# Optimization experiments

Hardware: AMD Instinct MI355X
Metric: run time of the kernel (lower is better)

Reference implementation:

```python
import jax, jax.numpy as jnp
import numpy as np

BITS = 4
MAXQ = 15           # 2**BITS - 1
PACK = 32 // BITS   # 8 nibbles per int32
GROUP = 128         # quantization group size along in_features


def _unpack_rows(packed, rows):
    """Unpack int32-packed 4-bit values along axis 0. packed: [Kp, N] -> [rows, N]."""
    shifts = jnp.arange(0, 32, BITS, dtype=jnp.int32)            # [PACK]
    u = (packed[:, None, :] >> shifts[None, :, None]) & MAXQ    # [Kp, PACK, N]
    return u.reshape(-1, packed.shape[1])[:rows]


def _unpack_cols(packed, cols):
    """Unpack int32-packed 4-bit values along axis 1. packed: [G, Np] -> [G, cols]."""
    shifts = jnp.arange(0, 32, BITS, dtype=jnp.int32)            # [PACK]
    u = (packed[:, :, None] >> shifts[None, None, :]) & MAXQ    # [G, Np, PACK]
    return u.reshape(packed.shape[0], -1)[:, :cols]


def setup_inputs() -> dict:
    key = jax.random.key(0)
    k1, k2, k3, k4, k5 = jax.random.split(key, 5)
    K, N = 4096, 11008
    x = jax.random.normal(k1, (4, 2048, K), dtype=jnp.float32)
    qweight = jax.random.randint(k2, (K // PACK, N), 0, 2**31 - 1, dtype=jnp.int32)
    scales = jax.random.uniform(k3, (K // GROUP, N), dtype=jnp.float32)
    qzeros = jax.random.randint(k4, (K // GROUP, (N + PACK - 1) // PACK), 0, 2**31 - 1, dtype=jnp.int32)
    bias = jax.random.normal(k5, (N,), dtype=jnp.float32)
    return {"x": x, "qweight": qweight, "scales": scales, "qzeros": qzeros, "bias": bias}


def reference(x, qweight, scales, qzeros, bias):
    K = x.shape[-1]
    N = scales.shape[1]
    qw = _unpack_rows(qweight, K)            # [K, N] int in [0, 15]
    qz = _unpack_cols(qzeros, N) + 1         # [G, N] int in [1, 16] (+1 per get_unpacked_params)
    s = jnp.repeat(scales, GROUP, axis=0)    # [K, N]  groupwise -> per-row
    z = jnp.repeat(qz, GROUP, axis=0)        # [K, N]
    W = (qw - z).astype(x.dtype) * s         # dequantized weight [K, N]
    out = jnp.matmul(x, W) + bias
    return out.astype(x.dtype)
```

## Files before the change

kernel.cpp:

```cpp
#include <hip/hip_runtime.h>
#include <hip/hip_bf16.h>
#include <stdint.h>

typedef __attribute__((ext_vector_type(4))) float f32x4;
typedef __attribute__((ext_vector_type(8))) short bf16x8;
typedef __attribute__((ext_vector_type(8))) unsigned short ushort8;
typedef __attribute__((ext_vector_type(4))) unsigned short ushort4v;

__device__ __forceinline__ unsigned short f2bf(float f) {
    union { float f; unsigned int u; } v; v.f = f;
    unsigned int u = v.u;
    u += 0x7FFFu + ((u >> 16) & 1u);
    return (unsigned short)(u >> 16);
}

__device__ __forceinline__ int swz(int row, int k) {
    return (row * 64 + k) ^ ((row & 7) << 3);
}

__device__ __forceinline__ void gld16(const void* g, void* l) {
    __builtin_amdgcn_global_load_lds(
        (const __attribute__((address_space(1))) unsigned int*)g,
        (__attribute__((address_space(3))) unsigned int*)l,
        16, 0, 0);
}

__global__ __launch_bounds__(256)
void prep(const float* __restrict__ X, const int* __restrict__ QW,
          const float* __restrict__ SC, const int* __restrict__ QZ,
          unsigned short* __restrict__ Xb, unsigned short* __restrict__ WT,
          int N, int K, long long n8, int deqB) {
    const int bid = blockIdx.x;
    const int t = threadIdx.x;
    if (bid < deqB) {
        const int ntiles = N >> 6;
        const int nb = bid % ntiles;
        const int kb = bid / ntiles;
        const int n0 = nb * 64, kp0 = kb * 64;
        #pragma unroll
        for (int w = 0; w < 16; ++w) {
            const int p = t + 256 * w;
            const int kpo = p & 63, ni = p >> 6;
            const int n = n0 + ni, kp = kp0 + kpo;
            const int g = kp >> 4;
            const float s = SC[(size_t)g * N + n];
            const int zq = ((QZ[(size_t)g * (N >> 3) + (n >> 3)] >> ((n & 7) * 4)) & 15) + 1;
            const float zb = -(float)zq * s;
            const unsigned int q = (unsigned int)QW[(size_t)kp * N + n];
            ushort8 o;
            #pragma unroll
            for (int j = 0; j < 8; ++j)
                o[j] = f2bf(fmaf((float)((q >> (4 * j)) & 15u), s, zb));
            *reinterpret_cast<ushort8*>(&WT[(size_t)n * K + kp * 8]) = o;
        }
    } else {
        long long i0 = (long long)(bid - deqB) * 256 + t;
        long long stride = (long long)(gridDim.x - deqB) * 256;
        for (long long i = i0; i < n8; i += stride) {
            const float4* p = reinterpret_cast<const float4*>(X + i * 8);
            float4 a = p[0], b = p[1];
            ushort8 o;
            o[0] = f2bf(a.x); o[1] = f2bf(a.y); o[2] = f2bf(a.z); o[3] = f2bf(a.w);
            o[4] = f2bf(b.x); o[5] = f2bf(b.y); o[6] = f2bf(b.z); o[7] = f2bf(b.w);
            *reinterpret_cast<ushort8*>(Xb + i * 8) = o;
        }
    }
}

__global__ __launch_bounds__(256)
void cvt_x(const float* __restrict__ X, unsigned short* __restrict__ Xb, long long n8) {
    long long i0 = (long long)blockIdx.x * 256 + threadIdx.x;
    long long stride = (long long)gridDim.x * 256;
    for (long long i = i0; i < n8; i += stride) {
        const float4* p = reinterpret_cast<const float4*>(X + i * 8);
        float4 a = p[0], b = p[1];
        ushort8 o;
        o[0] = f2bf(a.x); o[1] = f2bf(a.y); o[2] = f2bf(a.z); o[3] = f2bf(a.w);
        o[4] = f2bf(b.x); o[5] = f2bf(b.y); o[6] = f2bf(b.z); o[7] = f2bf(b.w);
        *reinterpret_cast<ushort8*>(Xb + i * 8) = o;
    }
}

__global__ __launch_bounds__(256)
void deq_w(const int* __restrict__ QW, const float* __restrict__ SC,
           const int* __restrict__ QZ, unsigned short* __restrict__ WT,
           int N, int K) {
    const int ntiles = N >> 6;
    const int nb = blockIdx.x % ntiles;
    const int kb = blockIdx.x / ntiles;
    const int n0 = nb * 64, kp0 = kb * 64;
    const int t = threadIdx.x;
    #pragma unroll
    for (int w = 0; w < 16; ++w) {
        const int p = t + 256 * w;
        const int kpo = p & 63, ni = p >> 6;
        const int n = n0 + ni, kp = kp0 + kpo;
        const int g = kp >> 4;
        const float s = SC[(size_t)g * N + n];
        const int zq = ((QZ[(size_t)g * (N >> 3) + (n >> 3)] >> ((n & 7) * 4)) & 15) + 1;
        const float zb = -(float)zq * s;
        const unsigned int q = (unsigned int)QW[(size_t)kp * N + n];
        ushort8 o;
        #pragma unroll
        for (int j = 0; j < 8; ++j)
            o[j] = f2bf(fmaf((float)((q >> (4 * j)) & 15u), s, zb));
        *reinterpret_cast<ushort8*>(&WT[(size_t)n * K + kp * 8]) = o;
    }
}

template<int KC, int NC>
__global__ __launch_bounds__(512, 2)
void qgemm_256(const unsigned short* __restrict__ Xb, const unsigned short* __restrict__ WT,
               const float* __restrict__ BIAS, float* __restrict__ OUT, int M) {
    __shared__ __align__(16) unsigned short S[65536];

    int id = blockIdx.x;
    const int nwg = gridDim.x;
    if ((nwg & 7) == 0) id = (id & 7) * (nwg >> 3) + (id >> 3);

    constexpr int ntn = NC >> 8;
    const int bm = (id / ntn) << 8;
    const int bn = (id % ntn) << 8;
    const int tid = threadIdx.x;
    const int lane = tid & 63;
    const int wid = tid >> 6;
    const int wm = (wid >> 2) * 64;
    const int wn = (wid & 3) * 32;
    const int lr = lane & 15;
    const int lk = (lane >> 4) * 8;

    const int xr  = (lr & 7) << 3;
    const int lo0 = lk ^ xr;
    const int lo1 = (32 + lk) ^ xr;
    const int lrow = lr * 64;

    f32x4 acc[8][4] = {};
    constexpr int nk = KC >> 6;

    const int srow = tid >> 3;
    const int scol = ((tid & 7) ^ (srow & 7)) << 3;
    const unsigned short* gA[2] = { Xb + (size_t)(bm + srow) * KC + scol,
                                    Xb + (size_t)(bm + 128 + srow) * KC + scol };
    const unsigned short* gB[2] = { WT + (size_t)(bn + srow) * KC + scol,
                                    WT + (size_t)(bn + 128 + srow) * KC + scol };

    auto stage = [&](int buf, int tt, int kind, int half) {
        const unsigned short* g = (kind ? gB[half] : gA[half]) + (size_t)tt * 64;
        unsigned short* lb = S + (kind ? 32768 : 0) + buf * 16384 + half * 8192 + tid * 8;
        gld16(g, lb);
        gld16(g + (size_t)64 * KC, lb + 4096);
    };

    bf16x8 aL[4][2], aH[4][2], bL[2][2], bH[2][2];

    auto loadA = [&](bf16x8 (&dst)[4][2], const unsigned short* Sa, int rbase) {
        const unsigned short* p = Sa + rbase * 64 + lrow;
        #pragma unroll
        for (int i = 0; i < 4; ++i) {
            dst[i][0] = *reinterpret_cast<const bf16x8*>(p + i * 1024 + lo0);
            dst[i][1] = *reinterpret_cast<const bf16x8*>(p + i * 1024 + lo1);
        }
    };
    auto loadB = [&](bf16x8 (&dst)[2][2], const unsigned short* Sb, int rbase) {
        const unsigned short* p = Sb + rbase * 64 + lrow;
        #pragma unroll
        for (int j = 0; j < 2; ++j) {
            dst[j][0] = *reinterpret_cast<const bf16x8*>(p + j * 1024 + lo0);
            dst[j][1] = *reinterpret_cast<const bf16x8*>(p + j * 1024 + lo1);
        }
    };
    auto quad = [&](bf16x8 (&A)[4][2], bf16x8 (&B)[2][2], int mi0, int nj0) {
        __builtin_amdgcn_s_setprio(1);
        #pragma unroll
        for (int kk = 0; kk < 2; ++kk)
            #pragma unroll
            for (int i = 0; i < 4; ++i)
                #pragma unroll
                for (int j = 0; j < 2; ++j)
                    acc[mi0 + i][nj0 + j] = __builtin_amdgcn_mfma_f32_16x16x32_bf16(
                        A[i][kk], B[j][kk], acc[mi0 + i][nj0 + j], 0, 0, 0);
        __builtin_amdgcn_s_setprio(0);
    };

    stage(0, 0, 0, 0); stage(0, 0, 0, 1);
    stage(0, 0, 1, 0); stage(0, 0, 1, 1);
    stage(1, 1, 0, 0); stage(1, 1, 1, 1); stage(1, 1, 0, 1);
    asm volatile("s_waitcnt vmcnt(6)" ::: "memory");

    for (int t = 0; t < nk; ++t) {
        const int c = t & 1;
        const unsigned short* Sa = S + c * 16384;
        const unsigned short* Sb = S + 32768 + c * 16384;

        if (t + 1 < nk) stage(c ^ 1, t + 1, 1, 0);

        __builtin_amdgcn_s_barrier();
        loadA(aL, Sa, wm);
        loadB(bL, Sb, wn);
        quad(aL, bL, 0, 0);
        __builtin_amdgcn_s_barrier();

        if (t + 2 < nk) stage(c, t + 2, 0, 0);
        loadB(bH, Sb, 128 + wn);
        quad(aL, bH, 0, 2);
        __builtin_amdgcn_s_barrier();

        if (t + 2 < nk) stage(c, t + 2, 1, 1);
        loadA(aH, Sa, 128 + wm);
        quad(aH, bL, 4, 0);
        __builtin_amdgcn_s_barrier();

        if (t + 2 < nk) {
            stage(c, t + 2, 0, 1);
            asm volatile("s_waitcnt vmcnt(6)" ::: "memory");
        } else {
            asm volatile("s_waitcnt vmcnt(0)" ::: "memory");
        }
        quad(aH, bH, 4, 2);
    }

    #pragma unroll
    for (int mi = 0; mi < 8; ++mi) {
        const int row = bm + wm + (mi & 3) * 16 + ((mi >> 2) ? 128 : 0) + (lane >> 4) * 4;
        #pragma unroll
        for (int nj = 0; nj < 4; ++nj) {
            const int col = bn + wn + (nj & 1) * 16 + ((nj >> 1) ? 128 : 0) + lr;
            const float b = BIAS[col];
            #pragma unroll
            for (int r = 0; r < 4; ++r)
                OUT[(size_t)(row + r) * NC + col] = acc[mi][nj][r] + b;
        }
    }
}

__global__ __launch_bounds__(256, 2)
void qgemm_ws(const unsigned short* __restrict__ Xb, const unsigned short* __restrict__ WT,
              const float* __restrict__ BIAS, float* __restrict__ OUT,
              int M, int N, int K) {
    __shared__ __align__(16) unsigned short As[2][128 * 64];
    __shared__ __align__(16) unsigned short Bs[2][128 * 64];

    const int ntn = N >> 7;
    const int bm = (blockIdx.x / ntn) * 128;
    const int bn = (blockIdx.x % ntn) * 128;
    const int tid = threadIdx.x;
    const int lane = tid & 63;
    const int wave = tid >> 6;
    const int wm = (wave >> 1) * 64, wn = (wave & 1) * 64;
    const int lr = lane & 15, lk = (lane >> 4) * 8;

    f32x4 acc[4][4] = {};
    const int nk = K >> 6;

    auto stage = [&](int buf, int t) {
        const int k0 = t * 64;
        #pragma unroll
        for (int p = 0; p < 4; ++p) {
            const int slot = p * 256 + tid;
            const int row = slot >> 3, c = slot & 7;
            const int gk = k0 + ((c ^ (row & 7)) << 3);
            gld16(Xb + (size_t)(bm + row) * K + gk, &As[buf][slot * 8]);
            gld16(WT + (size_t)(bn + row) * K + gk, &Bs[buf][slot * 8]);
        }
    };

    auto compute = [&](int buf) {
        #pragma unroll
        for (int kk = 0; kk < 2; ++kk) {
            bf16x8 af[4], bfr[4];
            #pragma unroll
            for (int i = 0; i < 4; ++i) {
                af[i]  = *reinterpret_cast<const bf16x8*>(&As[buf][swz(wm + i * 16 + lr, kk * 32 + lk)]);
                bfr[i] = *reinterpret_cast<const bf16x8*>(&Bs[buf][swz(wn + i * 16 + lr, kk * 32 + lk)]);
            }
            #pragma unroll
            for (int i = 0; i < 4; ++i)
                #pragma unroll
                for (int j = 0; j < 4; ++j)
                    acc[i][j] = __builtin_amdgcn_mfma_f32_16x16x32_bf16(af[i], bfr[j], acc[i][j], 0, 0, 0);
        }
    };

    stage(0, 0);
    __syncthreads();
    int cur = 0;
    for (int t = 0; t < nk; ++t) {
        if (t + 1 < nk) stage(cur ^ 1, t + 1);
        compute(cur);
        __syncthreads();
        cur ^= 1;
    }

    #pragma unroll
    for (int i = 0; i < 4; ++i) {
        #pragma unroll
        for (int j = 0; j < 4; ++j) {
            const int col = bn + wn + j * 16 + lr;
            const float b = BIAS[col];
            #pragma unroll
            for (int r = 0; r < 4; ++r) {
                const int row = bm + wm + i * 16 + (lane >> 4) * 4 + r;
                OUT[(size_t)row * N + col] = acc[i][j][r] + b;
            }
        }
    }
}

__global__ __launch_bounds__(256, 2)
void qgemm_fb(const float* __restrict__ X, const int* __restrict__ QW,
              const float* __restrict__ SC, const int* __restrict__ QZ,
              const float* __restrict__ BIAS, float* __restrict__ OUT,
              int M, int N, int K) {
    __shared__ __align__(16) unsigned short As[2][128 * 64];
    __shared__ __align__(16) unsigned short Bs[2][128 * 64];

    const int ntn = N / 128;
    const int bm = (blockIdx.x / ntn) * 128;
    const int bn = (blockIdx.x % ntn) * 128;
    const int tid  = threadIdx.x;
    const int lane = tid & 63;
    const int wave = tid >> 6;
    const int wm = (wave >> 1) * 64, wn = (wave & 1) * 64;
    const int lr = lane & 15, lk = (lane >> 4) * 8;
    const int a_c4 = tid & 15, a_r0 = tid >> 4;
    const int b_n  = tid & 127, b_k0 = tid >> 7;

    f32x4 acc[4][4] = {};
    float4 va[8];
    unsigned int wb[4];
    float sc_s = 0.f, sc_zb = 0.f;
    const int nk = K / 64;

    auto gload = [&](int t) {
        const int k0 = t * 64;
        #pragma unroll
        for (int p = 0; p < 8; ++p)
            va[p] = *reinterpret_cast<const float4*>(X + (size_t)(bm + a_r0 + p * 16) * K + k0 + a_c4 * 4);
        const int g  = k0 >> 7;
        const int gn = bn + b_n;
        sc_s = SC[(size_t)g * N + gn];
        const int zq = ((QZ[(size_t)g * (N >> 3) + (gn >> 3)] >> ((gn & 7) * 4)) & 15) + 1;
        sc_zb = -(float)zq * sc_s;
        #pragma unroll
        for (int p = 0; p < 4; ++p)
            wb[p] = (unsigned int)QW[(size_t)(t * 8 + b_k0 + p * 2) * N + gn];
    };

    auto lwrite = [&](int buf) {
        #pragma unroll
        for (int p = 0; p < 8; ++p) {
            const int row = a_r0 + p * 16;
            ushort4v b;
            b.x = f2bf(va[p].x); b.y = f2bf(va[p].y);
            b.z = f2bf(va[p].z); b.w = f2bf(va[p].w);
            *reinterpret_cast<ushort4v*>(&As[buf][swz(row, a_c4 * 4)]) = b;
        }
        #pragma unroll
        for (int p = 0; p < 4; ++p) {
            const int ko = b_k0 + p * 2;
            ushort8 o;
            #pragma unroll
            for (int j = 0; j < 8; ++j)
                o[j] = f2bf(fmaf((float)((wb[p] >> (4 * j)) & 15u), sc_s, sc_zb));
            *reinterpret_cast<ushort8*>(&Bs[buf][swz(b_n, ko * 8)]) = o;
        }
    };

    auto compute = [&](int buf) {
        #pragma unroll
        for (int kk = 0; kk < 2; ++kk) {
            bf16x8 af[4], bfr[4];
            #pragma unroll
            for (int i = 0; i < 4; ++i) {
                af[i]  = *reinterpret_cast<const bf16x8*>(&As[buf][swz(wm + i * 16 + lr, kk * 32 + lk)]);
                bfr[i] = *reinterpret_cast<const bf16x8*>(&Bs[buf][swz(wn + i * 16 + lr, kk * 32 + lk)]);
            }
            #pragma unroll
            for (int i = 0; i < 4; ++i)
                #pragma unroll
                for (int j = 0; j < 4; ++j)
                    acc[i][j] = __builtin_amdgcn_mfma_f32_16x16x32_bf16(af[i], bfr[j], acc[i][j], 0, 0, 0);
        }
    };

    gload(0); lwrite(0);
    __syncthreads();
    for (int t = 0; t < nk; ++t) {
        if (t + 1 < nk) gload(t + 1);
        compute(t & 1);
        if (t + 1 < nk) lwrite((t + 1) & 1);
        __syncthreads();
    }

    #pragma unroll
    for (int i = 0; i < 4; ++i) {
        #pragma unroll
        for (int j = 0; j < 4; ++j) {
            const int col = bn + wn + j * 16 + lr;
            const float b = BIAS[col];
            #pragma unroll
            for (int r = 0; r < 4; ++r) {
                const int row = bm + wm + i * 16 + (lane >> 4) * 4 + r;
                OUT[(size_t)row * N + col] = acc[i][j][r] + b;
            }
        }
    }
}

extern "C" void kernel_launch(void* const* d_in, const int* in_sizes, int n_in,
                              void* d_out, int out_size, void* d_ws, size_t ws_size,
                              hipStream_t stream) {
    const float* X    = (const float*)d_in[0];
    const int*   QW   = (const int*)d_in[1];
    const float* SC   = (const float*)d_in[2];
    const int*   QZ   = (const int*)d_in[3];
    const float* BIAS = (const float*)d_in[4];
    float* OUT = (float*)d_out;

    const int N = in_sizes[4];
    const long long qwsz = in_sizes[1];
    const int K = (int)(qwsz * 8 / N);
    const int M = in_sizes[0] / K;

    const size_t xb_bytes = (size_t)M * K * 2;
    const size_t wt_bytes = (size_t)N * K * 2;

    if (ws_size >= xb_bytes + wt_bytes) {
        unsigned short* Xb = (unsigned short*)d_ws;
        unsigned short* WT = Xb + (size_t)M * K;

        if (K == 4096 && N == 11008 && (M % 256) == 0) {
            const int deqB = (N >> 6) * (K / 512);
            prep<<<deqB + 2048, 256, 0, stream>>>(X, QW, SC, QZ, Xb, WT,
                                                  N, K, (long long)M * K / 8, deqB);
            qgemm_256<4096, 11008><<<(M / 256) * (11008 / 256), 512, 0, stream>>>(Xb, WT, BIAS, OUT, M);
        } else {
            cvt_x<<<2048, 256, 0, stream>>>(X, Xb, (long long)M * K / 8);
            deq_w<<<(N >> 6) * (K / 512), 256, 0, stream>>>(QW, SC, QZ, WT, N, K);
            qgemm_ws<<<(M / 128) * (N / 128), 256, 0, stream>>>(Xb, WT, BIAS, OUT, M, N, K);
        }
    } else {
        qgemm_fb<<<(M / 128) * (N / 128), 256, 0, stream>>>(X, QW, SC, QZ, BIAS, OUT, M, N, K);
    }
}
```

Baseline: 746.7 us.

## Switch 256x256 GEMM to 32x32x16 MFMA with new LDS swizzle

Replaces the 16x16x32 bf16 MFMA tiles with 32x32x16 MFMA tiles, giving each wave 4x2 accumulators of 16 floats instead of 8x4 of 4. The LDS staging layout and swizzle are reworked to pair rows so a lane can read 32-row fragments without bank conflicts. B-fragment loads and the second A load are moved earlier so LDS reads overlap the preceding MFMA block. The epilogue is rewritten for the 32x32 output layout. The goal is fewer MFMA issues and LDS reads per unit of work, at the cost of a new swizzle that could conflict or be subtly wrong.

```diff
diff --git a/kernel.cpp b/kernel.cpp
--- a/kernel.cpp
+++ b/kernel.cpp
@@ -3,6 +3,7 @@
 #include <stdint.h>
 
 typedef __attribute__((ext_vector_type(4))) float f32x4;
+typedef __attribute__((ext_vector_type(16))) float f32x16;
 typedef __attribute__((ext_vector_type(8))) short bf16x8;
 typedef __attribute__((ext_vector_type(8))) unsigned short ushort8;
 typedef __attribute__((ext_vector_type(4))) unsigned short ushort4v;
@@ -126,19 +127,22 @@
     const int wid = tid >> 6;
     const int wm = (wid >> 2) * 64;
     const int wn = (wid & 3) * 32;
-    const int lr = lane & 15;
-    const int lk = (lane >> 4) * 8;
-
-    const int xr  = (lr & 7) << 3;
-    const int lo0 = lk ^ xr;
-    const int lo1 = (32 + lk) ^ xr;
-    const int lrow = lr * 64;
-
-    f32x4 acc[8][4] = {};
+    const int l31 = lane & 31;
+    const int j0 = lane >> 5;
+
+    int offA0, s0A0, offA1, s0A1, offB0, s0B0;
+    {
+        int r0 = wm + l31;       offA0 = (r0 >> 1) * 128; s0A0 = ((r0 & 1) << 3) ^ ((r0 >> 1) & 15) ^ j0;
+        int r1 = wm + 32 + l31;  offA1 = (r1 >> 1) * 128; s0A1 = ((r1 & 1) << 3) ^ ((r1 >> 1) & 15) ^ j0;
+        int r2 = wn + l31;       offB0 = (r2 >> 1) * 128; s0B0 = ((r2 & 1) << 3) ^ ((r2 >> 1) & 15) ^ j0;
+    }
+
+    f32x16 acc[4][2] = {};
     constexpr int nk = KC >> 6;
 
-    const int srow = tid >> 3;
-    const int scol = ((tid & 7) ^ (srow & 7)) << 3;
+    const int u = (tid & 15) ^ ((tid >> 4) & 15);
+    const int srow = ((tid >> 4) << 1) | (u >> 3);
+    const int scol = (u & 7) << 3;
     const unsigned short* gA[2] = { Xb + (size_t)(bm + srow) * KC + scol,
                                     Xb + (size_t)(bm + 128 + srow) * KC + scol };
     const unsigned short* gB[2] = { WT + (size_t)(bn + srow) * KC + scol,
@@ -151,34 +155,28 @@
         gld16(g + (size_t)64 * KC, lb + 4096);
     };
 
-    bf16x8 aL[4][2], aH[4][2], bL[2][2], bH[2][2];
-
-    auto loadA = [&](bf16x8 (&dst)[4][2], const unsigned short* Sa, int rbase) {
-        const unsigned short* p = Sa + rbase * 64 + lrow;
-        #pragma unroll
-        for (int i = 0; i < 4; ++i) {
-            dst[i][0] = *reinterpret_cast<const bf16x8*>(p + i * 1024 + lo0);
-            dst[i][1] = *reinterpret_cast<const bf16x8*>(p + i * 1024 + lo1);
-        }
-    };
-    auto loadB = [&](bf16x8 (&dst)[2][2], const unsigned short* Sb, int rbase) {
-        const unsigned short* p = Sb + rbase * 64 + lrow;
-        #pragma unroll
-        for (int j = 0; j < 2; ++j) {
-            dst[j][0] = *reinterpret_cast<const bf16x8*>(p + j * 1024 + lo0);
-            dst[j][1] = *reinterpret_cast<const bf16x8*>(p + j * 1024 + lo1);
-        }
-    };
-    auto quad = [&](bf16x8 (&A)[4][2], bf16x8 (&B)[2][2], int mi0, int nj0) {
+    bf16x8 aL[2][4], aH[2][4], bL[4], bH[4];
+
+    auto loadApair = [&](bf16x8 (&dst)[2][4], const unsigned short* base) {
+        #pragma unroll
+        for (int kk = 0; kk < 4; ++kk) {
+            dst[0][kk] = *reinterpret_cast<const bf16x8*>(base + offA0 + ((s0A0 ^ (kk << 1)) << 3));
+            dst[1][kk] = *reinterpret_cast<const bf16x8*>(base + offA1 + ((s0A1 ^ (kk << 1)) << 3));
+        }
+    };
+    auto loadBv = [&](bf16x8 (&dst)[4], const unsigned short* base) {
+        #pragma unroll
+        for (int kk = 0; kk < 4; ++kk)
+            dst[kk] = *reinterpret_cast<const bf16x8*>(base + offB0 + ((s0B0 ^ (kk << 1)) << 3));
+    };
+    auto quad = [&](bf16x8 (&A)[2][4], bf16x8 (&B)[4], int m0, int nf) {
         __builtin_amdgcn_s_setprio(1);
         #pragma unroll
-        for (int kk = 0; kk < 2; ++kk)
-            #pragma unroll
-            for (int i = 0; i < 4; ++i)
-                #pragma unroll
-                for (int j = 0; j < 2; ++j)
-                    acc[mi0 + i][nj0 + j] = __builtin_amdgcn_mfma_f32_16x16x32_bf16(
-                        A[i][kk], B[j][kk], acc[mi0 + i][nj0 + j], 0, 0, 0);
+        for (int kk = 0; kk < 4; ++kk)
+            #pragma unroll
+            for (int m = 0; m < 2; ++m)
+                acc[m0 + m][nf] = __builtin_amdgcn_mfma_f32_32x32x16_bf16(
+                    A[m][kk], B[kk], acc[m0 + m][nf], 0, 0, 0);
         __builtin_amdgcn_s_setprio(0);
     };
 
@@ -195,40 +193,43 @@
         if (t + 1 < nk) stage(c ^ 1, t + 1, 1, 0);
 
         __builtin_amdgcn_s_barrier();
-        loadA(aL, Sa, wm);
-        loadB(bL, Sb, wn);
+        loadApair(aL, Sa);
+        loadBv(bL, Sb);
+        loadBv(bH, Sb + 8192);
         quad(aL, bL, 0, 0);
         __builtin_amdgcn_s_barrier();
 
         if (t + 2 < nk) stage(c, t + 2, 0, 0);
-        loadB(bH, Sb, 128 + wn);
-        quad(aL, bH, 0, 2);
+        quad(aL, bH, 0, 1);
+        loadApair(aH, Sa + 8192);
         __builtin_amdgcn_s_barrier();
 
         if (t + 2 < nk) stage(c, t + 2, 1, 1);
-        loadA(aH, Sa, 128 + wm);
-        quad(aH, bL, 4, 0);
+        quad(aH, bL, 2, 0);
         __builtin_amdgcn_s_barrier();
 
         if (t + 2 < nk) {
             stage(c, t + 2, 0, 1);
+            quad(aH, bH, 2, 1);
             asm volatile("s_waitcnt vmcnt(6)" ::: "memory");
         } else {
+            quad(aH, bH, 2, 1);
             asm volatile("s_waitcnt vmcnt(0)" ::: "memory");
         }
-        quad(aH, bH, 4, 2);
     }
 
     #pragma unroll
-    for (int mi = 0; mi < 8; ++mi) {
-        const int row = bm + wm + (mi & 3) * 16 + ((mi >> 2) ? 128 : 0) + (lane >> 4) * 4;
-        #pragma unroll
-        for (int nj = 0; nj < 4; ++nj) {
-            const int col = bn + wn + (nj & 1) * 16 + ((nj >> 1) ? 128 : 0) + lr;
-            const float b = BIAS[col];
-            #pragma unroll
-            for (int r = 0; r < 4; ++r)
-                OUT[(size_t)(row + r) * NC + col] = acc[mi][nj][r] + b;
+    for (int mf = 0; mf < 4; ++mf) {
+        const int rb = bm + (mf >> 1) * 128 + wm + (mf & 1) * 32 + (lane >> 5) * 4;
+        #pragma unroll
+        for (int nf = 0; nf < 2; ++nf) {
+            const int col = bn + nf * 128 + wn + l31;
+            const float bv = BIAS[col];
+            #pragma unroll
+            for (int q = 0; q < 4; ++q)
+                #pragma unroll
+                for (int r = 0; r < 4; ++r)
+                    OUT[(size_t)(rb + q * 8 + r) * NC + col] = acc[mf][nf][q * 4 + r] + bv;
         }
     }
 }
```

After: 813.7 us. 1.09x slower.
